# Kernel tuning notes

Hardware: AMD Instinct MI355X
Metric: run time of the kernel (lower is better)

The kernel has to match this reference:

```python
import jax, jax.numpy as jnp
import numpy as np

F_FRAMES = 128   # number of frames (seq_start_end rows)
P_PEDS = 32      # pedestrians per frame (uniform)
B = F_FRAMES * P_PEDS
E, H, BN, PM, M = 64, 128, 1024, 512, 1024
PRED_LEN = 12


def setup_inputs() -> dict:
    key = jax.random.key(0)
    ks = jax.random.split(key, 20)
    n = lambda k, s, sc=0.05: (jax.random.normal(k, s) * sc).astype(jnp.float32)
    starts = jnp.arange(F_FRAMES, dtype=jnp.int32) * P_PEDS
    seq_start_end = jnp.stack([starts, starts + P_PEDS], axis=1)
    return {
        "h0": n(ks[0], (1, B, H), 1.0),
        "c0": n(ks[1], (1, B, H), 1.0),
        "obs_final_pos": n(ks[2], (B, 2), 1.0),
        "obs_final_pos_rel": n(ks[3], (B, 2), 1.0),
        "W_emb": n(ks[4], (2, E)), "b_emb": jnp.zeros((E,), jnp.float32),
        "W_ih": n(ks[5], (4 * H, E)), "W_hh": n(ks[6], (4 * H, H)),
        "b_ih": jnp.zeros((4 * H,), jnp.float32), "b_hh": jnp.zeros((4 * H,), jnp.float32),
        "W_pos": n(ks[7], (H, 2)), "b_pos": jnp.zeros((2,), jnp.float32),
        "W_pe": n(ks[8], (2, E)), "b_pe": jnp.zeros((E,), jnp.float32),
        "W_p1": n(ks[9], (E + H, PM)), "b_p1": jnp.zeros((PM,), jnp.float32),
        "W_p2": n(ks[10], (PM, BN)), "b_p2": jnp.zeros((BN,), jnp.float32),
        "W_m1": n(ks[11], (H + BN, M)), "b_m1": jnp.zeros((M,), jnp.float32),
        "W_m2": n(ks[12], (M, H)), "b_m2": jnp.zeros((H,), jnp.float32),
        "seq_start_end": seq_start_end,
    }


def reference(h0, c0, obs_final_pos, obs_final_pos_rel,
              W_emb, b_emb, W_ih, W_hh, b_ih, b_hh, W_pos, b_pos,
              W_pe, b_pe, W_p1, b_p1, W_p2, b_p2, W_m1, b_m1, W_m2, b_m2,
              seq_start_end):
    Bn = h0.shape[1]
    F = seq_start_end.shape[0]
    P = Bn // F  # uniform frame size
    h, c = h0[0], c0[0]
    x0 = obs_final_pos_rel @ W_emb + b_emb  # decoder input embedding

    def step(carry, _):
        x, h, c, last_pos = carry
        # LSTM cell (PyTorch gate order i,f,g,o)
        gates = x @ W_ih.T + h @ W_hh.T + b_ih + b_hh  # (B, 4H)
        i, f, g, o = jnp.split(gates, 4, axis=-1)
        i, f, o = jax.nn.sigmoid(i), jax.nn.sigmoid(f), jax.nn.sigmoid(o)
        c_new = f * c + i * jnp.tanh(g)
        h_new = o * jnp.tanh(c_new)
        rel_pos = h_new @ W_pos + b_pos
        curr_pos = rel_pos + last_pos
        # PoolNet: per-frame pairwise rel-pos embed + MLP + max over neighbours j
        pos = curr_pos.reshape(F, P, 2)
        hf = h_new.reshape(F, P, H)
        rel = pos[:, None, :, :] - pos[:, :, None, :]  # rel[f,i,j] = pos_j - pos_i
        e = rel @ W_pe + b_pe  # (F,P,P,E)
        feat = jnp.concatenate(
            [e, jnp.broadcast_to(hf[:, None], (F, P, P, H))], axis=-1)  # h of j
        z = jax.nn.relu(feat @ W_p1 + b_p1)
        z = jax.nn.relu(z @ W_p2 + b_p2)  # (F,P,P,BN)
        pool_h = z.max(axis=2).reshape(Bn, BN)
        # hidden refresh MLP
        mi = jnp.concatenate([h_new, pool_h], axis=-1)
        nh = jax.nn.relu(mi @ W_m1 + b_m1)
        nh = jax.nn.relu(nh @ W_m2 + b_m2)
        x_new = rel_pos @ W_emb + b_emb
        return (x_new, nh, c_new, curr_pos), (curr_pos, rel_pos)

    _, (pred_seq, pred_seq_rel) = jax.lax.scan(
        jax.checkpoint(step), (x0, h, c, obs_final_pos), None, length=PRED_LEN)
    return pred_seq, pred_seq_rel
```

## Files before the change

kernel.cpp:

```cpp
#include <hip/hip_runtime.h>

#define NB 4096
#define HD 128
#define ED 64
#define NF 128
#define NP 32
#define TSTEPS 12

typedef __attribute__((ext_vector_type(8))) short short8;
typedef __attribute__((ext_vector_type(8))) __bf16 bf16x8;
typedef __attribute__((ext_vector_type(8))) _Float16 f16x8;
typedef __attribute__((ext_vector_type(4))) float f32x4;
typedef __attribute__((ext_vector_type(16))) float f32x16;

#define MFMA16(a, b, c)  __builtin_amdgcn_mfma_f32_16x16x32_bf16((a), (b), (c), 0, 0, 0)
#define MFMA32H(a, b, c) __builtin_amdgcn_mfma_f32_32x32x16_f16((a), (b), (c), 0, 0, 0)

__device__ __forceinline__ unsigned short f2bf(float f) {
  unsigned int x = __float_as_uint(f);
  x += 0x7fffu + ((x >> 16) & 1u);
  return (unsigned short)(x >> 16);
}

__device__ __forceinline__ float sigm(float x) { return 1.0f / (1.0f + expf(-x)); }

__device__ __forceinline__ f16x8 relu8(f16x8 x) {
  return __builtin_elementwise_max(x, (f16x8)(_Float16)0);
}


__global__ __launch_bounds__(256) void k_transpose_bf(const float* __restrict__ W,
                                                      unsigned short* __restrict__ Wt,
                                                      int K, int N) {
  __shared__ float t[32][33];
  int nb = blockIdx.x * 32, kb = blockIdx.y * 32;
  int tx = threadIdx.x & 31, ty = threadIdx.x >> 5;
  #pragma unroll
  for (int r = 0; r < 32; r += 8)
    t[ty + r][tx] = W[(size_t)(kb + ty + r) * N + nb + tx];
  __syncthreads();
  #pragma unroll
  for (int r = 0; r < 32; r += 8)
    Wt[(size_t)(nb + ty + r) * K + kb + tx] = f2bf(t[tx][ty + r]);
}

__global__ __launch_bounds__(256) void k_pack_bfrag32(const float* __restrict__ Wp2,
                                                      _Float16* __restrict__ Bf) {
  int U = blockIdx.x * 256 + threadIdx.x;
  int l = U & 63, cb = (U >> 6) & 31, ks = U >> 11;
  int col = cb * 32 + (l & 31);
  int k0 = ks * 16 + (l >> 5) * 8;
  f16x8 r;
  #pragma unroll
  for (int e = 0; e < 8; ++e) r[e] = (_Float16)Wp2[(size_t)(k0 + e) * 1024 + col];
  *(f16x8*)(Bf + (size_t)U * 8) = r;
}

__global__ __launch_bounds__(256) void k_pack_lstm_w(const float* __restrict__ Wih,
                                                     const float* __restrict__ Whh,
                                                     float* __restrict__ WihT,
                                                     float* __restrict__ WhhT) {
  int idx = blockIdx.x * 256 + threadIdx.x;
  if (idx < 64 * 512) { int k = idx >> 9, n = idx & 511; WihT[idx] = Wih[n * 64 + k]; }
  if (idx < 128 * 512) { int k = idx >> 9, n = idx & 511; WhhT[idx] = Whh[n * 128 + k]; }
}

__global__ __launch_bounds__(256) void k_pack_wpp(const float* __restrict__ Wpe,
                                                  const float* __restrict__ bpe,
                                                  const float* __restrict__ Wp1,
                                                  const float* __restrict__ bp1,
                                                  float* __restrict__ Wpp,
                                                  float* __restrict__ cvec) {
  int n = blockIdx.x * 256 + threadIdx.x;
  if (n >= 512) return;
  float s0 = 0.f, s1 = 0.f, sc = 0.f;
  for (int k = 0; k < 64; ++k) {
    float w = Wp1[k * 512 + n];
    s0 += Wpe[k] * w;
    s1 += Wpe[64 + k] * w;
    sc += bpe[k] * w;
  }
  Wpp[n * 2] = s0; Wpp[n * 2 + 1] = s1; cvec[n] = sc + bp1[n];
}

__global__ __launch_bounds__(256) void k_x0(const float* __restrict__ ofr,
                                            const float* __restrict__ Wemb,
                                            const float* __restrict__ bemb,
                                            float* __restrict__ x) {
  int idx = blockIdx.x * 256 + threadIdx.x;
  if (idx >= NB * ED) return;
  int row = idx >> 6, e = idx & 63;
  x[idx] = bemb[e] + ofr[row * 2] * Wemb[e] + ofr[row * 2 + 1] * Wemb[64 + e];
}


__global__ __launch_bounds__(256) void k12_lstm_uv(
    const float* __restrict__ x, const float* __restrict__ hin, const float* __restrict__ cin,
    const float* __restrict__ WihT, const float* __restrict__ WhhT,
    const float* __restrict__ bih, const float* __restrict__ bhh,
    const float* __restrict__ Wpos, const float* __restrict__ bpos,
    const float* __restrict__ Wemb, const float* __restrict__ bemb,
    const float* __restrict__ lastpos,
    const float* __restrict__ Wp1, const float* __restrict__ Wpp,
    const float* __restrict__ cvec,
    float* __restrict__ cout, unsigned short* __restrict__ mi,
    float* __restrict__ posout, float* __restrict__ xout,
    float* __restrict__ outc, float* __restrict__ outr,
    _Float16* __restrict__ u16, _Float16* __restrict__ v16) {
  __shared__ float xh[8][192];
  __shared__ float hnl[8][128];
  __shared__ float rp[8][2];
  __shared__ float cp[8][2];
  int tid = threadIdx.x;
  int r0 = blockIdx.x * 8;
  for (int idx = tid; idx < 8 * 192; idx += 256) {
    int r = idx / 192, k = idx % 192;
    xh[r][k] = (k < 64) ? x[(r0 + r) * 64 + k] : hin[(r0 + r) * 128 + (k - 64)];
  }
  __syncthreads();
  int j = tid & 127, rg = tid >> 7;
  float acc0[4], acc1[4], acc2[4], acc3[4];
  {
    float b0 = bih[j] + bhh[j];
    float b1 = bih[128 + j] + bhh[128 + j];
    float b2 = bih[256 + j] + bhh[256 + j];
    float b3 = bih[384 + j] + bhh[384 + j];
    #pragma unroll
    for (int r = 0; r < 4; ++r) { acc0[r] = b0; acc1[r] = b1; acc2[r] = b2; acc3[r] = b3; }
  }
  for (int k = 0; k < 64; ++k) {
    float w0 = WihT[k * 512 + j], w1 = WihT[k * 512 + 128 + j],
          w2 = WihT[k * 512 + 256 + j], w3 = WihT[k * 512 + 384 + j];
    #pragma unroll
    for (int r = 0; r < 4; ++r) {
      float xv = xh[rg * 4 + r][k];
      acc0[r] += w0 * xv; acc1[r] += w1 * xv; acc2[r] += w2 * xv; acc3[r] += w3 * xv;
    }
  }
  for (int k = 0; k < 128; ++k) {
    float w0 = WhhT[k * 512 + j], w1 = WhhT[k * 512 + 128 + j],
          w2 = WhhT[k * 512 + 256 + j], w3 = WhhT[k * 512 + 384 + j];
    #pragma unroll
    for (int r = 0; r < 4; ++r) {
      float hv = xh[rg * 4 + r][64 + k];
      acc0[r] += w0 * hv; acc1[r] += w1 * hv; acc2[r] += w2 * hv; acc3[r] += w3 * hv;
    }
  }
  #pragma unroll
  for (int r = 0; r < 4; ++r) {
    int row = r0 + rg * 4 + r;
    float ig = sigm(acc0[r]), fg = sigm(acc1[r]), gg = tanhf(acc2[r]), og = sigm(acc3[r]);
    float cn = fg * cin[row * 128 + j] + ig * gg;
    float hv = og * tanhf(cn);
    cout[row * 128 + j] = cn;
    mi[(size_t)row * 1152 + j] = f2bf(hv);
    hnl[rg * 4 + r][j] = hv;
  }
  __syncthreads();
  {
    int r = tid >> 5;
    int d = (tid >> 4) & 1;
    int l = tid & 15;
    float s = 0.f;
    #pragma unroll
    for (int k = l; k < 128; k += 16) s += hnl[r][k] * Wpos[k * 2 + d];
    s += __shfl_xor(s, 1);
    s += __shfl_xor(s, 2);
    s += __shfl_xor(s, 4);
    s += __shfl_xor(s, 8);
    if (l == 0) {
      int row = r0 + r;
      float rel = s + bpos[d];
      float cur = rel + lastpos[row * 2 + d];
      rp[r][d] = rel;
      cp[r][d] = cur;
      posout[row * 2 + d] = cur;
      outc[row * 2 + d] = cur;
      outr[row * 2 + d] = rel;
    }
  }
  __syncthreads();
  for (int idx = tid; idx < 8 * 64; idx += 256) {
    int r = idx >> 6, e = idx & 63;
    xout[(r0 + r) * 64 + e] = bemb[e] + rp[r][0] * Wemb[e] + rp[r][1] * Wemb[64 + e];
  }
  int n = tid, n2 = tid + 256;
  float aA[8], aB[8];
  #pragma unroll
  for (int r = 0; r < 8; ++r) { aA[r] = 0.f; aB[r] = 0.f; }
  for (int k = 0; k < 128; ++k) {
    float wA = Wp1[(64 + k) * 512 + n], wB = Wp1[(64 + k) * 512 + n2];
    #pragma unroll
    for (int r = 0; r < 8; ++r) { aA[r] += wA * hnl[r][k]; aB[r] += wB * hnl[r][k]; }
  }
  float wp0A = Wpp[n * 2], wp1A = Wpp[n * 2 + 1], cA = cvec[n];
  float wp0B = Wpp[n2 * 2], wp1B = Wpp[n2 * 2 + 1], cB = cvec[n2];
  #pragma unroll
  for (int r = 0; r < 8; ++r) {
    int row = r0 + r;
    float t0 = cp[r][0] * wp0A + cp[r][1] * wp1A;
    v16[(size_t)row * 512 + n] = (_Float16)t0;
    u16[(size_t)row * 512 + n] = (_Float16)(t0 + aA[r] + cA);
    float t1 = cp[r][0] * wp0B + cp[r][1] * wp1B;
    v16[(size_t)row * 512 + n2] = (_Float16)t1;
    u16[(size_t)row * 512 + n2] = (_Float16)(t1 + aB[r] + cB);
  }
}

__global__ __launch_bounds__(256, 2) void k3_pool(
    const _Float16* __restrict__ u16, const _Float16* __restrict__ v16,
    const _Float16* __restrict__ Bf, const float* __restrict__ bp2,
    unsigned short* __restrict__ mi) {
  __shared__ _Float16 u_lds[32 * 512];
  __shared__ _Float16 v_lds[4 * 512];
  int f = blockIdx.x, ig = blockIdx.y, ng = blockIdx.z;
  int tid = threadIdx.x, wid = tid >> 6, lane = tid & 63;
  int r32 = lane & 31, hi = lane >> 5;
  int ip = wid >> 1, nh = wid & 1;

  const f16x8* Bfu = (const f16x8*)Bf;
  int cb0 = ng * 8 + nh * 4;

  f16x8 Bb[4][4];
  #pragma unroll
  for (int nt = 0; nt < 4; ++nt) Bb[0][nt] = Bfu[(size_t)((0 * 32 + cb0 + nt) * 64 + lane)];
  #pragma unroll
  for (int nt = 0; nt < 4; ++nt) Bb[1][nt] = Bfu[(size_t)((1 * 32 + cb0 + nt) * 64 + lane)];

  #pragma unroll
  for (int t = 0; t < 8; ++t) {
    int unit = tid + t * 256;
    int row = unit >> 6, seg = unit & 63;
    f16x8 val = *(const f16x8*)(u16 + (size_t)(f * 32 + row) * 512 + seg * 8);
    int byte = (row << 10) + (seg << 4);
    byte ^= (row & 7) << 4;
    *(f16x8*)((char*)u_lds + byte) = val;
  }
  {
    int row = tid >> 6, seg = tid & 63;
    *(f16x8*)(v_lds + (row << 9) + seg * 8) =
        *(const f16x8*)(v16 + (size_t)(f * 32 + ig * 4 + row) * 512 + seg * 8);
  }
  __syncthreads();

  f32x16 acc[2][4];
  #pragma unroll
  for (int a = 0; a < 2; ++a)
    #pragma unroll
    for (int n = 0; n < 4; ++n)
      #pragma unroll
      for (int r = 0; r < 16; ++r) acc[a][n][r] = 0.f;

  int ubase = (r32 << 10) + (hi << 4);
  int usw = (r32 & 7) << 4;
  const _Float16* vp0 = v_lds + ((ip * 2 + 0) << 9) + hi * 8;
  const _Float16* vp1 = vp0 + 512;

#define K3STEP(KS, CUR, NXT, KLOAD)                                              \
  {                                                                              \
    if ((KLOAD) < 32) {                                                          \
      _Pragma("unroll")                                                          \
      for (int nt = 0; nt < 4; ++nt)                                             \
        Bb[NXT][nt] = Bfu[(size_t)(((KLOAD) * 32 + cb0 + nt) * 64 + lane)];      \
    }                                                                            \
    f16x8 uf = *(const f16x8*)((const char*)u_lds + ((ubase + (KS) * 32) ^ usw));\
    f16x8 vv0 = *(const f16x8*)(vp0 + (KS) * 16);                                \
    f16x8 vv1 = *(const f16x8*)(vp1 + (KS) * 16);                                \
    f16x8 a0 = relu8(uf - vv0);                                                  \
    f16x8 a1 = relu8(uf - vv1);                                                  \
    __builtin_amdgcn_s_setprio(1);                                               \
    _Pragma("unroll")                                                            \
    for (int nt = 0; nt < 4; ++nt) {                                             \
      acc[0][nt] = MFMA32H(a0, Bb[CUR][nt], acc[0][nt]);                         \
      acc[1][nt] = MFMA32H(a1, Bb[CUR][nt], acc[1][nt]);                         \
    }                                                                            \
    __builtin_amdgcn_s_setprio(0);                                               \
  }

  #pragma unroll
  for (int kk = 0; kk < 32; kk += 4) {
    K3STEP(kk + 0, 0, 2, kk + 2)
    K3STEP(kk + 1, 1, 3, kk + 3)
    K3STEP(kk + 2, 2, 0, kk + 4)
    K3STEP(kk + 3, 3, 1, kk + 5)
  }
#undef K3STEP

  #pragma unroll
  for (int ii = 0; ii < 2; ++ii) {
    int rowg = f * 32 + ig * 4 + ip * 2 + ii;
    #pragma unroll
    for (int nt = 0; nt < 4; ++nt) {
      float m = acc[ii][nt][0];
      #pragma unroll
      for (int r = 1; r < 16; ++r) m = fmaxf(m, acc[ii][nt][r]);
      m = fmaxf(m, __shfl_xor(m, 32));
      if (hi == 0) {
        int col = (cb0 + nt) * 32 + r32;
        float val = fmaxf(m + bp2[col], 0.f);
        mi[(size_t)rowg * 1152 + 128 + col] = f2bf(val);
      }
    }
  }
}

__global__ __launch_bounds__(512) void k4_mlp1(
    const unsigned short* __restrict__ mi, const unsigned short* __restrict__ Wt,
    const float* __restrict__ bm1, unsigned short* __restrict__ nh1) {
  int bid = blockIdx.x;
  int mb = bid & 63, nb = bid >> 6;
  int tid = threadIdx.x, wid = tid >> 6, lane = tid & 63;
  int row0 = mb * 64 + (wid >> 2) * 32;
  int nc0 = nb * 256 + (wid & 3) * 64;
  int c = lane & 15, q = lane >> 4;
  const unsigned short* a0p = mi + (size_t)(row0 + c) * 1152;
  const unsigned short* a1p = a0p + 16 * 1152;
  const unsigned short* bb = Wt + (size_t)(nc0 + c) * 1152;
  f32x4 acc[2][4];
  #pragma unroll
  for (int a = 0; a < 2; ++a)
    #pragma unroll
    for (int b = 0; b < 4; ++b) acc[a][b] = (f32x4){0.f, 0.f, 0.f, 0.f};
  for (int ks = 0; ks < 36; ++ks) {
    int k0 = ks * 32 + q * 8;
    bf16x8 a0 = *(const bf16x8*)(a0p + k0);
    bf16x8 a1 = *(const bf16x8*)(a1p + k0);
    #pragma unroll
    for (int nt = 0; nt < 4; ++nt) {
      bf16x8 bf = *(const bf16x8*)(bb + (size_t)nt * 16 * 1152 + k0);
      acc[0][nt] = MFMA16(a0, bf, acc[0][nt]);
      acc[1][nt] = MFMA16(a1, bf, acc[1][nt]);
    }
  }
  #pragma unroll
  for (int mt = 0; mt < 2; ++mt)
    #pragma unroll
    for (int nt = 0; nt < 4; ++nt)
      #pragma unroll
      for (int r = 0; r < 4; ++r) {
        int row = row0 + mt * 16 + q * 4 + r;
        int col = nc0 + nt * 16 + c;
        float val = fmaxf(acc[mt][nt][r] + bm1[col], 0.f);
        nh1[(size_t)row * 1024 + col] = f2bf(val);
      }
}

__global__ __launch_bounds__(128) void k5_mlp2(
    const unsigned short* __restrict__ nh1, const unsigned short* __restrict__ Wt,
    const float* __restrict__ bm2, float* __restrict__ hout) {
  int bid = blockIdx.x;
  int tid = threadIdx.x, wid = tid >> 6, lane = tid & 63;
  int row0 = bid * 16;
  int nc0 = wid * 64;
  int c = lane & 15, q = lane >> 4;
  const unsigned short* ap = nh1 + (size_t)(row0 + c) * 1024;
  const unsigned short* bb = Wt + (size_t)(nc0 + c) * 1024;
  f32x4 acc[4];
  #pragma unroll
  for (int b = 0; b < 4; ++b) acc[b] = (f32x4){0.f, 0.f, 0.f, 0.f};
  for (int ks = 0; ks < 32; ++ks) {
    int k0 = ks * 32 + q * 8;
    bf16x8 a = *(const bf16x8*)(ap + k0);
    #pragma unroll
    for (int nt = 0; nt < 4; ++nt) {
      bf16x8 bf = *(const bf16x8*)(bb + (size_t)nt * 16 * 1024 + k0);
      acc[nt] = MFMA16(a, bf, acc[nt]);
    }
  }
  #pragma unroll
  for (int nt = 0; nt < 4; ++nt)
    #pragma unroll
    for (int r = 0; r < 4; ++r) {
      int row = row0 + q * 4 + r;
      int col = nc0 + nt * 16 + c;
      hout[(size_t)row * 128 + col] = fmaxf(acc[nt][r] + bm2[col], 0.f);
    }
}


extern "C" void kernel_launch(void* const* d_in, const int* in_sizes, int n_in,
                              void* d_out, int out_size, void* d_ws, size_t ws_size,
                              hipStream_t stream) {
  const float* h0   = (const float*)d_in[0];
  const float* c0   = (const float*)d_in[1];
  const float* ofp  = (const float*)d_in[2];
  const float* ofr  = (const float*)d_in[3];
  const float* Wemb = (const float*)d_in[4];
  const float* bemb = (const float*)d_in[5];
  const float* Wih  = (const float*)d_in[6];
  const float* Whh  = (const float*)d_in[7];
  const float* bih  = (const float*)d_in[8];
  const float* bhh  = (const float*)d_in[9];
  const float* Wpos = (const float*)d_in[10];
  const float* bpos = (const float*)d_in[11];
  const float* Wpe  = (const float*)d_in[12];
  const float* bpe  = (const float*)d_in[13];
  const float* Wp1  = (const float*)d_in[14];
  const float* bp1  = (const float*)d_in[15];
  const float* Wp2  = (const float*)d_in[16];
  const float* bp2  = (const float*)d_in[17];
  const float* Wm1  = (const float*)d_in[18];
  const float* bm1  = (const float*)d_in[19];
  const float* Wm2  = (const float*)d_in[20];
  const float* bm2  = (const float*)d_in[21];

  char* ws = (char*)d_ws;
  size_t off = 0;
  auto alloc = [&](size_t bytes) {
    char* p = ws + off;
    off += (bytes + 255) & ~(size_t)255;
    return p;
  };
  float* h    = (float*)alloc((size_t)NB * HD * 4);
  float* cst  = (float*)alloc((size_t)NB * HD * 4);
  float* xbuf = (float*)alloc((size_t)NB * ED * 4);
  float* pos  = (float*)alloc((size_t)NB * 2 * 4);
  _Float16* u16 = (_Float16*)alloc((size_t)NB * 512 * 2);
  _Float16* v16 = (_Float16*)alloc((size_t)NB * 512 * 2);
  unsigned short* mi   = (unsigned short*)alloc((size_t)NB * 1152 * 2);
  unsigned short* nh1  = (unsigned short*)alloc((size_t)NB * 1024 * 2);
  float* WihT = (float*)alloc(64 * 512 * 4);
  float* WhhT = (float*)alloc(128 * 512 * 4);
  float* Wpp  = (float*)alloc(512 * 2 * 4);
  float* cvec = (float*)alloc(512 * 4);
  _Float16* Bf  = (_Float16*)alloc((size_t)1024 * 512 * 2);
  unsigned short* Wm1t = (unsigned short*)alloc((size_t)1024 * 1152 * 2);
  unsigned short* Wm2t = (unsigned short*)alloc((size_t)128 * 1024 * 2);

  float* outc = (float*)d_out;
  float* outr = outc + (size_t)TSTEPS * NB * 2;

  k_pack_lstm_w<<<256, 256, 0, stream>>>(Wih, Whh, WihT, WhhT);
  k_pack_wpp<<<2, 256, 0, stream>>>(Wpe, bpe, Wp1, bp1, Wpp, cvec);
  k_pack_bfrag32<<<256, 256, 0, stream>>>(Wp2, Bf);
  k_transpose_bf<<<dim3(1024 / 32, 1152 / 32), 256, 0, stream>>>(Wm1, Wm1t, 1152, 1024);
  k_transpose_bf<<<dim3(128 / 32, 1024 / 32), 256, 0, stream>>>(Wm2, Wm2t, 1024, 128);
  k_x0<<<NB * ED / 256, 256, 0, stream>>>(ofr, Wemb, bemb, xbuf);

  for (int t = 0; t < TSTEPS; ++t) {
    const float* hin = (t == 0) ? h0 : h;
    const float* cin = (t == 0) ? c0 : cst;
    const float* lp  = (t == 0) ? ofp : pos;
    k12_lstm_uv<<<NB / 8, 256, 0, stream>>>(xbuf, hin, cin, WihT, WhhT, bih, bhh,
                                            Wpos, bpos, Wemb, bemb, lp, Wp1, Wpp, cvec,
                                            cst, mi, pos, xbuf,
                                            outc + (size_t)t * NB * 2,
                                            outr + (size_t)t * NB * 2, u16, v16);
    k3_pool<<<dim3(128, 8, 4), 256, 0, stream>>>(u16, v16, Bf, bp2, mi);
    k4_mlp1<<<256, 512, 0, stream>>>(mi, Wm1t, bm1, nh1);
    k5_mlp2<<<256, 128, 0, stream>>>(nh1, Wm2t, bm2, h);
  }
}
```

Measured before the change: 2.846 ms.

## Retile pool kernel to 4 rows x 2 column tiles per wave with deeper B prefetch

Each wave in the pooling kernel now handles 4 query pedestrians and 2 output column tiles instead of 2 and 4, and each block covers 8 pedestrians. The grid changes to (128, 4, 8) to match. One u fragment read from LDS is now reused across four relu-differences, which cuts LDS traffic and elementwise work per MFMA. The B-fragment register prefetch goes from 2 steps ahead to 7 steps ahead, better hiding global load latency. The cost is that each B fragment is reused by fewer rows per load, the v LDS buffer doubles, and register pressure rises.

```diff
diff --git a/kernel.cpp b/kernel.cpp
--- a/kernel.cpp
+++ b/kernel.cpp
@@ -212,20 +212,21 @@
     const _Float16* __restrict__ Bf, const float* __restrict__ bp2,
     unsigned short* __restrict__ mi) {
   __shared__ _Float16 u_lds[32 * 512];
-  __shared__ _Float16 v_lds[4 * 512];
+  __shared__ _Float16 v_lds[8 * 512];
   int f = blockIdx.x, ig = blockIdx.y, ng = blockIdx.z;
   int tid = threadIdx.x, wid = tid >> 6, lane = tid & 63;
   int r32 = lane & 31, hi = lane >> 5;
   int ip = wid >> 1, nh = wid & 1;
 
   const f16x8* Bfu = (const f16x8*)Bf;
-  int cb0 = ng * 8 + nh * 4;
-
-  f16x8 Bb[4][4];
-  #pragma unroll
-  for (int nt = 0; nt < 4; ++nt) Bb[0][nt] = Bfu[(size_t)((0 * 32 + cb0 + nt) * 64 + lane)];
-  #pragma unroll
-  for (int nt = 0; nt < 4; ++nt) Bb[1][nt] = Bfu[(size_t)((1 * 32 + cb0 + nt) * 64 + lane)];
+  int cb0 = ng * 4 + nh * 2;
+
+  f16x8 Bb[8][2];
+  #pragma unroll
+  for (int s = 0; s < 7; ++s) {
+    Bb[s][0] = Bfu[(size_t)((s * 32 + cb0 + 0) * 64 + lane)];
+    Bb[s][1] = Bfu[(size_t)((s * 32 + cb0 + 1) * 64 + lane)];
+  }
 
   #pragma unroll
   for (int t = 0; t < 8; ++t) {
@@ -236,61 +237,62 @@
     byte ^= (row & 7) << 4;
     *(f16x8*)((char*)u_lds + byte) = val;
   }
-  {
-    int row = tid >> 6, seg = tid & 63;
+  #pragma unroll
+  for (int t = 0; t < 2; ++t) {
+    int unit = tid + t * 256;
+    int row = unit >> 6, seg = unit & 63;
     *(f16x8*)(v_lds + (row << 9) + seg * 8) =
-        *(const f16x8*)(v16 + (size_t)(f * 32 + ig * 4 + row) * 512 + seg * 8);
+        *(const f16x8*)(v16 + (size_t)(f * 32 + ig * 8 + row) * 512 + seg * 8);
   }
   __syncthreads();
 
-  f32x16 acc[2][4];
-  #pragma unroll
-  for (int a = 0; a < 2; ++a)
-    #pragma unroll
-    for (int n = 0; n < 4; ++n)
+  f32x16 acc[4][2];
+  #pragma unroll
+  for (int a = 0; a < 4; ++a)
+    #pragma unroll
+    for (int n = 0; n < 2; ++n)
       #pragma unroll
       for (int r = 0; r < 16; ++r) acc[a][n][r] = 0.f;
 
   int ubase = (r32 << 10) + (hi << 4);
   int usw = (r32 & 7) << 4;
-  const _Float16* vp0 = v_lds + ((ip * 2 + 0) << 9) + hi * 8;
-  const _Float16* vp1 = vp0 + 512;
-
-#define K3STEP(KS, CUR, NXT, KLOAD)                                              \
+  const _Float16* vp = v_lds + ((ip * 4) << 9) + hi * 8;
+
+#define K3STEP(KS)                                                               \
   {                                                                              \
-    if ((KLOAD) < 32) {                                                          \
-      _Pragma("unroll")                                                          \
-      for (int nt = 0; nt < 4; ++nt)                                             \
-        Bb[NXT][nt] = Bfu[(size_t)(((KLOAD) * 32 + cb0 + nt) * 64 + lane)];      \
+    if ((KS) + 7 < 32) {                                                         \
+      Bb[((KS) + 7) & 7][0] = Bfu[(size_t)((((KS) + 7) * 32 + cb0 + 0) * 64 + lane)]; \
+      Bb[((KS) + 7) & 7][1] = Bfu[(size_t)((((KS) + 7) * 32 + cb0 + 1) * 64 + lane)]; \
     }                                                                            \
     f16x8 uf = *(const f16x8*)((const char*)u_lds + ((ubase + (KS) * 32) ^ usw));\
-    f16x8 vv0 = *(const f16x8*)(vp0 + (KS) * 16);                                \
-    f16x8 vv1 = *(const f16x8*)(vp1 + (KS) * 16);                                \
-    f16x8 a0 = relu8(uf - vv0);                                                  \
-    f16x8 a1 = relu8(uf - vv1);                                                  \
+    f16x8 a0 = relu8(uf - *(const f16x8*)(vp + (KS) * 16));                      \
+    f16x8 a1 = relu8(uf - *(const f16x8*)(vp + 512 + (KS) * 16));                \
+    f16x8 a2 = relu8(uf - *(const f16x8*)(vp + 1024 + (KS) * 16));               \
+    f16x8 a3 = relu8(uf - *(const f16x8*)(vp + 1536 + (KS) * 16));               \
     __builtin_amdgcn_s_setprio(1);                                               \
-    _Pragma("unroll")                                                            \
-    for (int nt = 0; nt < 4; ++nt) {                                             \
-      acc[0][nt] = MFMA32H(a0, Bb[CUR][nt], acc[0][nt]);                         \
-      acc[1][nt] = MFMA32H(a1, Bb[CUR][nt], acc[1][nt]);                         \
-    }                                                                            \
+    acc[0][0] = MFMA32H(a0, Bb[(KS) & 7][0], acc[0][0]);                         \
+    acc[1][0] = MFMA32H(a1, Bb[(KS) & 7][0], acc[1][0]);                         \
+    acc[2][0] = MFMA32H(a2, Bb[(KS) & 7][0], acc[2][0]);                         \
+    acc[3][0] = MFMA32H(a3, Bb[(KS) & 7][0], acc[3][0]);                         \
+    acc[0][1] = MFMA32H(a0, Bb[(KS) & 7][1], acc[0][1]);                         \
+    acc[1][1] = MFMA32H(a1, Bb[(KS) & 7][1], acc[1][1]);                         \
+    acc[2][1] = MFMA32H(a2, Bb[(KS) & 7][1], acc[2][1]);                         \
+    acc[3][1] = MFMA32H(a3, Bb[(KS) & 7][1], acc[3][1]);                         \
     __builtin_amdgcn_s_setprio(0);                                               \
   }
 
   #pragma unroll
-  for (int kk = 0; kk < 32; kk += 4) {
-    K3STEP(kk + 0, 0, 2, kk + 2)
-    K3STEP(kk + 1, 1, 3, kk + 3)
-    K3STEP(kk + 2, 2, 0, kk + 4)
-    K3STEP(kk + 3, 3, 1, kk + 5)
+  for (int kk = 0; kk < 32; kk += 8) {
+    K3STEP(kk + 0) K3STEP(kk + 1) K3STEP(kk + 2) K3STEP(kk + 3)
+    K3STEP(kk + 4) K3STEP(kk + 5) K3STEP(kk + 6) K3STEP(kk + 7)
   }
 #undef K3STEP
 
   #pragma unroll
-  for (int ii = 0; ii < 2; ++ii) {
-    int rowg = f * 32 + ig * 4 + ip * 2 + ii;
-    #pragma unroll
-    for (int nt = 0; nt < 4; ++nt) {
+  for (int ii = 0; ii < 4; ++ii) {
+    int rowg = f * 32 + ig * 8 + ip * 4 + ii;
+    #pragma unroll
+    for (int nt = 0; nt < 2; ++nt) {
       float m = acc[ii][nt][0];
       #pragma unroll
       for (int r = 1; r < 16; ++r) m = fmaxf(m, acc[ii][nt][r]);
@@ -446,7 +448,7 @@
                                             cst, mi, pos, xbuf,
                                             outc + (size_t)t * NB * 2,
                                             outr + (size_t)t * NB * 2, u16, v16);
-    k3_pool<<<dim3(128, 8, 4), 256, 0, stream>>>(u16, v16, Bf, bp2, mi);
+    k3_pool<<<dim3(128, 4, 8), 256, 0, stream>>>(u16, v16, Bf, bp2, mi);
     k4_mlp1<<<256, 512, 0, stream>>>(mi, Wm1t, bm1, nh1);
     k5_mlp2<<<256, 128, 0, stream>>>(nh1, Wm2t, bm2, h);
   }
```

Result: no change. 2.883 ms (+1.3%).
